# Optimization experiments

Measured on AMD Instinct MI355X. Metric: run time of the kernel, lower is better.

## Reference

```python
import jax, jax.numpy as jnp
import numpy as np

WS = 7   # window size
SS = 3   # shift size
NH = 8   # num heads


def _rel_pos_index(ws):
    coords = np.stack(np.meshgrid(np.arange(ws), np.arange(ws), indexing='ij')).reshape(2, -1)
    rel = (coords[:, :, None] - coords[:, None, :]).transpose(1, 2, 0)  # (N,N,2)
    rel[..., 0] += ws - 1
    rel[..., 1] += ws - 1
    rel[..., 0] *= 2 * ws - 1
    return rel.sum(-1)  # (N,N) int


def _shift_attn_mask(hp, wp, ws, ss):
    img = np.zeros((hp, wp), dtype=np.float32)
    sl = (slice(0, -ws), slice(-ws, -ss), slice(-ss, None))
    cnt = 0
    for hs in sl:
        for vs in sl:
            img[hs, vs] = cnt
            cnt += 1
    mw = img.reshape(hp // ws, ws, wp // ws, ws).transpose(0, 2, 1, 3).reshape(-1, ws * ws)
    diff = mw[:, None, :] - mw[:, :, None]  # (nW,N,N)
    return np.where(diff != 0, -100.0, 0.0).astype(np.float32)


def _window_partition(x, ws):
    b, h, w, c = x.shape
    x = x.reshape(b, h // ws, ws, w // ws, ws, c).transpose(0, 1, 3, 2, 4, 5)
    return x.reshape(-1, ws * ws, c)


def _window_reverse(win, h, w, ws, b):
    c = win.shape[-1]
    x = win.reshape(b, h // ws, w // ws, ws, ws, c).transpose(0, 1, 3, 2, 4, 5)
    return x.reshape(b, h, w, c)


def setup_inputs() -> dict:
    key = jax.random.key(0)
    ks = jax.random.split(key, 6)
    B, H, W, C = 16, 56, 56, 256
    return {
        'query': jax.random.normal(ks[0], (B, H * W, C), jnp.float32),
        'w_qkv': jax.random.normal(ks[1], (C, 3 * C), jnp.float32) * 0.02,
        'b_qkv': jax.random.normal(ks[2], (3 * C,), jnp.float32) * 0.02,
        'w_proj': jax.random.normal(ks[3], (C, C), jnp.float32) * 0.02,
        'b_proj': jax.random.normal(ks[4], (C,), jnp.float32) * 0.02,
        'rel_bias_table': jax.random.normal(ks[5], ((2 * WS - 1) ** 2, NH), jnp.float32) * 0.02,
        'height': H,
        'width': W,
    }


def reference(query, w_qkv, b_qkv, w_proj, b_proj, rel_bias_table, height, width):
    B, L, C = query.shape
    ws, ss, nh = WS, SS, NH
    hd = C // nh
    scale = hd ** -0.5
    x = query.reshape(B, height, width, C)

    pad_b = (ws - height % ws) % ws
    pad_r = (ws - width % ws) % ws
    x = jnp.pad(x, ((0, 0), (0, pad_b), (0, pad_r), (0, 0)))
    hp, wp = height + pad_b, width + pad_r

    # cyclic shift
    x = jnp.roll(x, (-ss, -ss), axis=(1, 2))
    attn_mask = jnp.asarray(_shift_attn_mask(hp, wp, ws, ss))  # (nW,N,N)

    win = _window_partition(x, ws)  # (B*nW, N, C)
    BW, N, _ = win.shape
    nW = (hp // ws) * (wp // ws)

    qkv = (win @ w_qkv + b_qkv).reshape(BW, N, 3, nh, hd).transpose(2, 0, 3, 1, 4)
    q, k, v = qkv[0], qkv[1], qkv[2]  # (BW, nh, N, hd)

    attn = jnp.einsum('bhnd,bhmd->bhnm', q * scale, k)  # (BW,nh,N,N)
    bias = rel_bias_table[_rel_pos_index(ws).reshape(-1)].reshape(N, N, nh).transpose(2, 0, 1)
    attn = attn + bias[None]
    attn = attn.reshape(B, nW, nh, N, N) + attn_mask[None, :, None]
    attn = jax.nn.softmax(attn.reshape(BW, nh, N, N), axis=-1)

    out = jnp.einsum('bhnm,bhmd->bhnd', attn, v).transpose(0, 2, 1, 3).reshape(BW, N, C)
    out = out @ w_proj + b_proj

    x = _window_reverse(out, hp, wp, ws, B)
    x = jnp.roll(x, (ss, ss), axis=(1, 2))
    x = x[:, :height, :width, :]
    return x.reshape(B, height * width, C)
```

## Files before the change

### kernel.cpp

```cpp
#include <hip/hip_runtime.h>


#define IMG 56
#define SCALE 0.17677669529663687f

typedef unsigned short u16;
typedef unsigned int u32;
typedef unsigned long long u64;
typedef __attribute__((ext_vector_type(8))) short short8;
typedef __attribute__((ext_vector_type(4))) float floatx4;

__device__ __forceinline__ float bflo(u32 u) { return __uint_as_float(u << 16); }
__device__ __forceinline__ u16 f2bf(float f) {
  u32 u = __float_as_uint(f);
  return (u16)((u + 0x7fffu + ((u >> 16) & 1u)) >> 16);
}
__device__ __forceinline__ u32 cvt2(float lo, float hi) {
  u32 r;
  __asm__("v_cvt_pk_bf16_f32 %0, %1, %2" : "=v"(r) : "v"(lo), "v"(hi));
  return r;
}
__device__ __forceinline__ short8 pack8(float4 lo, float4 hi) {
  union { u32 u[4]; short8 s; } r;
  r.u[0] = cvt2(lo.x, lo.y); r.u[1] = cvt2(lo.z, lo.w);
  r.u[2] = cvt2(hi.x, hi.y); r.u[3] = cvt2(hi.z, hi.w);
  return r.s;
}
#define MFMA(a, b, c) __builtin_amdgcn_mfma_f32_16x16x32_bf16(a, b, c, 0, 0, 0)

__device__ __forceinline__ void gll16(const void* g, const void* l) {
  __builtin_amdgcn_global_load_lds(
      (const __attribute__((address_space(1))) void*)g,
      (__attribute__((address_space(3))) void*)l, 16, 0, 0);
}
#define FENCE_VM() __asm__ volatile("s_waitcnt vmcnt(0)" ::: "memory")
#define FENCE_LGKM() __asm__ volatile("s_waitcnt lgkmcnt(0)" ::: "memory")

__device__ __forceinline__ int xcd_swizzle(int orig, int nwg) {
  int q = nwg >> 3, r = nwg & 7;
  int xcd = orig & 7, loc = orig >> 3;
  return (xcd < r ? xcd * (q + 1) : r * (q + 1) + (xcd - r) * q) + loc;
}

__global__ __launch_bounds__(256) void convert_kernel(
    const float* __restrict__ w_qkv, const float* __restrict__ w_proj,
    const float* __restrict__ bias_table, u16* __restrict__ zpad,
    u16* __restrict__ Wtq, u16* __restrict__ Wtp, u16* __restrict__ biasM) {
  int t = blockIdx.x * 256 + threadIdx.x;
  if (t < 196608) {
    int n = t % 768, k = t / 768;
    Wtq[n * 256 + k] = f2bf(w_qkv[t]);
  } else if (t < 262144) {
    int u = t - 196608;
    int n = u & 255, k = u >> 8;
    Wtp[n * 256 + k] = f2bf(w_proj[u]);
  } else if (t < 262272) {
    zpad[t - 262144] = 0;
  } else if (t < 393344) {
    int idx = t - 262272;
    int type = idx >> 15;
    int r = idx & 32767;
    int h = r >> 12, mt = (r >> 10) & 3, quad = (r >> 8) & 3;
    int l15 = (r >> 4) & 15, nt = (r >> 2) & 3, reg = r & 3;
    int row = 16 * mt + 4 * quad + reg;
    int col = 16 * nt + l15;
    float v;
    if (col >= 49) v = -1e30f;
    else if (row >= 49) v = 0.f;
    else {
      int yn = row / 7, xn = row - yn * 7;
      int ym = col / 7, xm = col - ym * 7;
      v = bias_table[((yn - ym + 6) * 13 + (xn - xm + 6)) * 8 + h];
      int bndH = (type >> 1) & 1, bndV = type & 1;
      int rc = (bndH ? ((yn < 4) ? 1 : 2) : 0) * 3 + (bndV ? ((xn < 4) ? 1 : 2) : 0);
      int cc = (bndH ? ((ym < 4) ? 1 : 2) : 0) * 3 + (bndV ? ((xm < 4) ? 1 : 2) : 0);
      if (rc != cc) v -= 100.f;
    }
    biasM[idx] = f2bf(v);
  }
}

__global__ __launch_bounds__(256) void qkv_gemm(
    const float* __restrict__ query, const u16* __restrict__ Wtq,
    const float* __restrict__ b_qkv, u16* __restrict__ QKVb,
    int img0, int Mrows, int mtiles) {
  union LU {
    struct { u16 As[128][64]; u16 Bs[128][64]; } s;
    u16 Cs[128][144];
  };
  __shared__ LU L;
  __shared__ float bqs[128];
  const int tid = threadIdx.x;
  const int wgid = xcd_swizzle(blockIdx.x, mtiles * 6);
  const int n0 = (wgid % 6) << 7;
  const int m0 = (wgid / 6) << 7;
  const int lane = tid & 63, w = tid >> 6;
  const int l15 = lane & 15, quad = lane >> 4;
  const int mq = w & 1, nq = w >> 1;
  if (tid < 128) bqs[tid] = b_qkv[n0 + tid];

  const float* qsrc[4];
  const u16* wsrc[4];
  #pragma unroll
  for (int c = 0; c < 4; ++c) {
    int e = (w * 4 + c) * 64 + lane;
    int row = e >> 3, sp = e & 7, sub = sp ^ (row & 7);
    int gr = m0 + row; if (gr >= Mrows) gr = 0;
    int winl = gr / 49, tok = gr - winl * 49;
    int bL = winl >> 6, wi = (winl >> 3) & 7, wj = winl & 7;
    int pr = tok / 7, pc = tok - pr * 7;
    int y = wi * 7 + pr + 3; if (y >= IMG) y -= IMG;
    int x = wj * 7 + pc + 3; if (x >= IMG) x -= IMG;
    qsrc[c] = query + (((size_t)((img0 + bL) * 3136 + y * IMG + x)) << 8) + sub * 8;
    wsrc[c] = Wtq + (size_t)(n0 + row) * 256 + sub * 8;
  }

  const floatx4 z4 = {0.f, 0.f, 0.f, 0.f};
  floatx4 acc[4][4];
  #pragma unroll
  for (int i = 0; i < 4; ++i)
    #pragma unroll
    for (int j = 0; j < 4; ++j) acc[i][j] = z4;

  float4 a0[4], a1[4];
  #pragma unroll
  for (int c = 0; c < 4; ++c) {
    a0[c] = reinterpret_cast<const float4*>(qsrc[c])[0];
    a1[c] = reinterpret_cast<const float4*>(qsrc[c])[1];
  }

  for (int ki = 0; ki < 4; ++ki) {
    const int k0 = ki * 64;
    __syncthreads();
    #pragma unroll
    for (int c = 0; c < 4; ++c)
      gll16(wsrc[c] + k0, (const char*)&L.s.Bs[0][0] + (w * 4 + c) * 1024);
    #pragma unroll
    for (int c = 0; c < 4; ++c) {
      short8 pk = pack8(a0[c], a1[c]);
      *reinterpret_cast<short8*>(
          (char*)&L.s.As[0][0] + (w * 4 + c) * 1024 + lane * 16) = pk;
    }
    FENCE_VM();
    __syncthreads();
    {
      const int kn = (ki < 3) ? k0 + 64 : 0;
      #pragma unroll
      for (int c = 0; c < 4; ++c) {
        const float* src = qsrc[c] + kn;
        a0[c] = reinterpret_cast<const float4*>(src)[0];
        a1[c] = reinterpret_cast<const float4*>(src)[1];
      }
    }
    #pragma unroll
    for (int ks = 0; ks < 2; ++ks) {
      short8 af[4], bfv[4];
      #pragma unroll
      for (int mt = 0; mt < 4; ++mt) {
        int r = 64 * mq + 16 * mt + l15;
        af[mt] = *reinterpret_cast<const short8*>(
            &L.s.As[r][((4 * ks + quad) ^ (l15 & 7)) * 8]);
      }
      #pragma unroll
      for (int nt = 0; nt < 4; ++nt) {
        int r = 64 * nq + 16 * nt + l15;
        bfv[nt] = *reinterpret_cast<const short8*>(
            &L.s.Bs[r][((4 * ks + quad) ^ (l15 & 7)) * 8]);
      }
      #pragma unroll
      for (int mt = 0; mt < 4; ++mt)
        #pragma unroll
        for (int nt = 0; nt < 4; ++nt)
          acc[mt][nt] = MFMA(af[mt], bfv[nt], acc[mt][nt]);
    }
  }
  __syncthreads();
  #pragma unroll
  for (int mt = 0; mt < 4; ++mt)
    #pragma unroll
    for (int nt = 0; nt < 4; ++nt) {
      float bias = bqs[64 * nq + 16 * nt + l15];
      #pragma unroll
      for (int reg = 0; reg < 4; ++reg) {
        int row = 64 * mq + 16 * mt + 4 * quad + reg;
        int col = 64 * nq + 16 * nt + l15;
        L.Cs[row][col] = f2bf(acc[mt][nt][reg] + bias);
      }
    }
  __syncthreads();
  int r = tid >> 1, half = tid & 1;
  if (m0 + r < Mrows) {
    u16* dst = QKVb + (size_t)(m0 + r) * 768 + n0 + half * 64;
    const u16* src = &L.Cs[r][half * 64];
    #pragma unroll
    for (int it = 0; it < 8; ++it)
      reinterpret_cast<uint4*>(dst)[it] = reinterpret_cast<const uint4*>(src)[it];
  }
}

__global__ __launch_bounds__(256) void attn_kernel(
    const u16* __restrict__ QKVb, const u16* __restrict__ biasM,
    const u16* __restrict__ zpad, u16* __restrict__ O) {
  __shared__ __align__(16) u16 wbuf[4][6144];
  const int tid = threadIdx.x;
  const int winl = blockIdx.x >> 1;
  const int hg = (blockIdx.x & 1) * 4;
  const int lane = tid & 63, w = tid >> 6;
  const int l15 = lane & 15, quad = lane >> 4;
  const int h = hg + w;
  const int wi = (winl >> 3) & 7;
  const int wj = winl & 7;
  const int type = ((wi == 7) ? 2 : 0) | ((wj == 7) ? 1 : 0);

  u16* wb = wbuf[w];
  const size_t wrow = (size_t)winl * 49;
  #pragma unroll
  for (int c = 0; c < 4; ++c) {
    int tok = c * 16 + (lane >> 2), sub = lane & 3;
    const u16 *gq, *gk;
    if (tok < 49) {
      const u16* g = QKVb + (wrow + tok) * 768 + h * 32 + sub * 8;
      gq = g; gk = g + 256;
    } else {
      gq = zpad + sub * 8; gk = zpad + sub * 8;
    }
    gll16(gq, (const char*)wb + c * 1024);
    gll16(gk, (const char*)wb + 4096 + c * 1024);
  }
  short8 v0 = {}, v1 = {}, v2 = {}, v3 = {};
  {
    int tok = lane;
    if (tok < 49) {
      const short8* g = reinterpret_cast<const short8*>(
          QKVb + (wrow + tok) * 768 + 512 + h * 32);
      v0 = g[0]; v1 = g[1]; v2 = g[2]; v3 = g[3];
    }
  }
  const u16* bb = biasM + ((((type << 3) + h) << 12) + (quad << 8) + (l15 << 4));
  short8 bf0[4], bf1[4];
  #pragma unroll
  for (int mt = 0; mt < 4; ++mt) {
    bf0[mt] = *reinterpret_cast<const short8*>(bb + (mt << 10));
    bf1[mt] = *reinterpret_cast<const short8*>(bb + (mt << 10) + 8);
  }
  {
    int tok = lane;
    #pragma unroll
    for (int d = 0; d < 8; ++d) {
      wb[4096 + (d     ) * 64 + tok] = (u16)v0[d];
      wb[4096 + (d +  8) * 64 + tok] = (u16)v1[d];
      wb[4096 + (d + 16) * 64 + tok] = (u16)v2[d];
      wb[4096 + (d + 24) * 64 + tok] = (u16)v3[d];
    }
  }
  FENCE_VM(); FENCE_LGKM();

  const floatx4 z4 = {0.f, 0.f, 0.f, 0.f};
  short8 qf[4], kf[4];
  #pragma unroll
  for (int mt = 0; mt < 4; ++mt)
    qf[mt] = *reinterpret_cast<const short8*>(&wb[(16 * mt + l15) * 32 + quad * 8]);
  #pragma unroll
  for (int nt = 0; nt < 4; ++nt)
    kf[nt] = *reinterpret_cast<const short8*>(&wb[2048 + (16 * nt + l15) * 32 + quad * 8]);
  floatx4 sc[4][4];
  #pragma unroll
  for (int mt = 0; mt < 4; ++mt)
    #pragma unroll
    for (int nt = 0; nt < 4; ++nt) sc[mt][nt] = MFMA(qf[mt], kf[nt], z4);

  #pragma unroll
  for (int mt = 0; mt < 4; ++mt)
    #pragma unroll
    for (int nt = 0; nt < 4; ++nt)
      #pragma unroll
      for (int reg = 0; reg < 4; ++reg) {
        u16 bv = (nt < 2) ? (u16)bf0[mt][(nt << 2) | reg]
                          : (u16)bf1[mt][((nt & 1) << 2) | reg];
        sc[mt][nt][reg] = sc[mt][nt][reg] * SCALE + bflo((u32)bv);
      }
  #pragma unroll
  for (int mt = 0; mt < 4; ++mt)
    #pragma unroll
    for (int reg = 0; reg < 4; ++reg) {
      float m = fmaxf(fmaxf(sc[mt][0][reg], sc[mt][1][reg]),
                      fmaxf(sc[mt][2][reg], sc[mt][3][reg]));
      m = fmaxf(m, __shfl_xor(m, 1)); m = fmaxf(m, __shfl_xor(m, 2));
      m = fmaxf(m, __shfl_xor(m, 4)); m = fmaxf(m, __shfl_xor(m, 8));
      float sum = 0.f;
      #pragma unroll
      for (int nt = 0; nt < 4; ++nt) {
        float e = __expf(sc[mt][nt][reg] - m);
        sc[mt][nt][reg] = e; sum += e;
      }
      sum += __shfl_xor(sum, 1); sum += __shfl_xor(sum, 2);
      sum += __shfl_xor(sum, 4); sum += __shfl_xor(sum, 8);
      float inv = 1.f / sum;
      #pragma unroll
      for (int nt = 0; nt < 4; ++nt) sc[mt][nt][reg] *= inv;
    }
  #pragma unroll
  for (int mt = 0; mt < 4; ++mt)
    #pragma unroll
    for (int nt = 0; nt < 4; ++nt)
      #pragma unroll
      for (int reg = 0; reg < 4; ++reg)
        wb[(16 * mt + 4 * quad + reg) * 64 + 16 * nt + l15] = f2bf(sc[mt][nt][reg]);
  FENCE_LGKM();
  floatx4 oa[4][2];
  #pragma unroll
  for (int mt = 0; mt < 4; ++mt) { oa[mt][0] = z4; oa[mt][1] = z4; }
  #pragma unroll
  for (int ks = 0; ks < 2; ++ks) {
    short8 pf[4], vf[2];
    #pragma unroll
    for (int mt = 0; mt < 4; ++mt)
      pf[mt] = *reinterpret_cast<const short8*>(
          &wb[(16 * mt + l15) * 64 + ks * 32 + quad * 8]);
    #pragma unroll
    for (int ntl = 0; ntl < 2; ++ntl)
      vf[ntl] = *reinterpret_cast<const short8*>(
          &wb[4096 + (16 * ntl + l15) * 64 + ks * 32 + quad * 8]);
    #pragma unroll
    for (int mt = 0; mt < 4; ++mt)
      #pragma unroll
      for (int ntl = 0; ntl < 2; ++ntl)
        oa[mt][ntl] = MFMA(pf[mt], vf[ntl], oa[mt][ntl]);
  }
  FENCE_LGKM();
  #pragma unroll
  for (int mt = 0; mt < 4; ++mt)
    #pragma unroll
    for (int ntl = 0; ntl < 2; ++ntl)
      #pragma unroll
      for (int reg = 0; reg < 4; ++reg)
        wb[4096 + (16 * mt + 4 * quad + reg) * 32 + 16 * ntl + l15] =
            f2bf(oa[mt][ntl][reg]);
  FENCE_LGKM();
  #pragma unroll
  for (int c = 0; c < 4; ++c) {
    int slot = c * 64 + lane;
    if (slot < 196) {
      int tok = slot >> 2, sub = slot & 3;
      uint4 v = *reinterpret_cast<const uint4*>(&wb[4096 + tok * 32 + sub * 8]);
      *reinterpret_cast<uint4*>(O + (wrow + tok) * 256 + h * 32 + sub * 8) = v;
    }
  }
}

__global__ __launch_bounds__(256) void proj_gemm(
    const u16* __restrict__ O, const u16* __restrict__ Wtp,
    const float* __restrict__ b_proj, float* __restrict__ out,
    int img0, int Mrows, int mtiles) {
  union LU {
    struct { u16 As[128][64]; u16 Bs[128][64]; } s;
    float Cs[64][132];
  };
  __shared__ LU L;
  __shared__ float bps[128];
  const int tid = threadIdx.x;
  const int wgid = xcd_swizzle(blockIdx.x, mtiles * 2);
  const int n0 = (wgid & 1) << 7;
  const int m0 = (wgid >> 1) << 7;
  const int lane = tid & 63, w = tid >> 6;
  const int l15 = lane & 15, quad = lane >> 4;
  const int mq = w & 1, nq = w >> 1;
  if (tid < 128) bps[tid] = b_proj[n0 + tid];

  const floatx4 z4 = {0.f, 0.f, 0.f, 0.f};
  floatx4 acc[4][4];
  #pragma unroll
  for (int i = 0; i < 4; ++i)
    #pragma unroll
    for (int j = 0; j < 4; ++j) acc[i][j] = z4;

  for (int ki = 0; ki < 4; ++ki) {
    const int k0 = ki * 64;
    __syncthreads();
    #pragma unroll
    for (int c = 0; c < 4; ++c) {
      int e = (w * 4 + c) * 64 + lane;
      int row = e >> 3, sp = e & 7, sub = sp ^ (row & 7);
      int gr = m0 + row; if (gr >= Mrows) gr = 0;
      gll16(O + (size_t)gr * 256 + k0 + sub * 8,
            (const char*)&L.s.As[0][0] + (w * 4 + c) * 1024);
      gll16(Wtp + (size_t)(n0 + row) * 256 + k0 + sub * 8,
            (const char*)&L.s.Bs[0][0] + (w * 4 + c) * 1024);
    }
    FENCE_VM();
    __syncthreads();
    #pragma unroll
    for (int ks = 0; ks < 2; ++ks) {
      short8 af[4], bfv[4];
      #pragma unroll
      for (int mt = 0; mt < 4; ++mt) {
        int r = 64 * mq + 16 * mt + l15;
        af[mt] = *reinterpret_cast<const short8*>(
            &L.s.As[r][((4 * ks + quad) ^ (l15 & 7)) * 8]);
      }
      #pragma unroll
      for (int nt = 0; nt < 4; ++nt) {
        int r = 64 * nq + 16 * nt + l15;
        bfv[nt] = *reinterpret_cast<const short8*>(
            &L.s.Bs[r][((4 * ks + quad) ^ (l15 & 7)) * 8]);
      }
      #pragma unroll
      for (int mt = 0; mt < 4; ++mt)
        #pragma unroll
        for (int nt = 0; nt < 4; ++nt)
          acc[mt][nt] = MFMA(af[mt], bfv[nt], acc[mt][nt]);
    }
  }
  #pragma unroll
  for (int mh = 0; mh < 2; ++mh) {
    __syncthreads();
    if (mq == mh) {
      #pragma unroll
      for (int nt = 0; nt < 4; ++nt) {
        float bias = bps[64 * nq + 16 * nt + l15];
        #pragma unroll
        for (int mt = 0; mt < 4; ++mt)
          #pragma unroll
          for (int reg = 0; reg < 4; ++reg)
            L.Cs[16 * mt + 4 * quad + reg][64 * nq + 16 * nt + l15] =
                acc[mt][nt][reg] + bias;
      }
    }
    __syncthreads();
    int r = tid >> 2, seg = tid & 3;
    int gr = m0 + mh * 64 + r;
    if (gr < Mrows) {
      u32 winl = (u32)gr / 49u;
      int tok = gr - (int)winl * 49;
      int bL = winl >> 6, wi = (winl >> 3) & 7, wj = winl & 7;
      int pr = tok / 7, pc = tok - pr * 7;
      int y = wi * 7 + pr + 3; if (y >= IMG) y -= IMG;
      int x = wj * 7 + pc + 3; if (x >= IMG) x -= IMG;
      float* op = out + (((size_t)((img0 + bL) * 3136 + y * IMG + x)) << 8) +
                  n0 + seg * 32;
      const float* src = &L.Cs[r][seg * 32];
      #pragma unroll
      for (int i = 0; i < 8; ++i)
        reinterpret_cast<float4*>(op)[i] = reinterpret_cast<const float4*>(src)[i];
    }
  }
}

extern "C" void kernel_launch(void* const* d_in, const int* in_sizes, int n_in,
                              void* d_out, int out_size, void* d_ws, size_t ws_size,
                              hipStream_t stream) {
  const float* query      = (const float*)d_in[0];
  const float* w_qkv      = (const float*)d_in[1];
  const float* b_qkv      = (const float*)d_in[2];
  const float* w_proj     = (const float*)d_in[3];
  const float* b_proj     = (const float*)d_in[4];
  const float* bias_table = (const float*)d_in[5];

  u16* wsu   = (u16*)d_ws;
  u16* zpad  = wsu;
  u16* Wtq   = wsu + 128;
  u16* Wtp   = wsu + 196736;
  u16* biasM = wsu + 262272;

  int P = 16;
  while (P > 1 && 2ull * (393344ull + (u64)P * 3211264ull) > (u64)ws_size) P >>= 1;
  u16* QKVb = wsu + 393344;
  u16* Ob   = QKVb + (size_t)P * 2408448;
  const int npass  = 16 / P;
  const int Mrows  = P * 3136;
  const int mtiles = (Mrows + 127) / 128;

  convert_kernel<<<1537, 256, 0, stream>>>(w_qkv, w_proj, bias_table,
                                           zpad, Wtq, Wtp, biasM);
  for (int p = 0; p < npass; ++p) {
    qkv_gemm<<<mtiles * 6, 256, 0, stream>>>(query, Wtq, b_qkv, QKVb,
                                             p * P, Mrows, mtiles);
    attn_kernel<<<P * 128, 256, 0, stream>>>(QKVb, biasM, zpad, Ob);
    proj_gemm<<<mtiles * 2, 256, 0, stream>>>(Ob, Wtp, b_proj, (float*)d_out,
                                              p * P, Mrows, mtiles);
  }
}
```

Before: 223.9 us.

## Double-buffer LDS tiles in QKV and projection GEMMs to overlap loads with MFMA

Both GEMM kernels now keep two LDS stages for the A and B tiles. The next K-slice is issued via global_load_lds (plus the packed fp32-to-bf16 query tile) before the MFMAs on the current slice run, with explicit waitcnt and raw s_barrier in place of two __syncthreads per iteration. The aim is to hide global load latency behind the matrix math. The cost is double the LDS footprint, which may lower occupancy, and hand-tuned vmcnt values that must match the exact number of outstanding loads.

Measured after the change: 226.7 us. Within noise of the previous version (+1.2%).

```diff
diff --git a/kernel.cpp b/kernel.cpp
--- a/kernel.cpp
+++ b/kernel.cpp
@@ -35,6 +35,12 @@
 }
 #define FENCE_VM() __asm__ volatile("s_waitcnt vmcnt(0)" ::: "memory")
 #define FENCE_LGKM() __asm__ volatile("s_waitcnt lgkmcnt(0)" ::: "memory")
+#define WAIT_VM8_LGKM0() \
+  __asm__ volatile("s_waitcnt vmcnt(8) lgkmcnt(0)" ::: "memory")
+#define WAIT_VM0_LGKM0() \
+  __asm__ volatile("s_waitcnt vmcnt(0) lgkmcnt(0)" ::: "memory")
+#define RAW_BARRIER() __asm__ volatile("s_barrier" ::: "memory")
+#define SCHED0() __builtin_amdgcn_sched_barrier(0)
 
 __device__ __forceinline__ int xcd_swizzle(int orig, int nwg) {
   int q = nwg >> 3, r = nwg & 7;
@@ -85,7 +91,7 @@
     const float* __restrict__ b_qkv, u16* __restrict__ QKVb,
     int img0, int Mrows, int mtiles) {
   union LU {
-    struct { u16 As[128][64]; u16 Bs[128][64]; } s;
+    struct { u16 As[2][128][64]; u16 Bs[2][128][64]; } s;
     u16 Cs[128][144];
   };
   __shared__ LU L;
@@ -114,6 +120,7 @@
     qsrc[c] = query + (((size_t)((img0 + bL) * 3136 + y * IMG + x)) << 8) + sub * 8;
     wsrc[c] = Wtq + (size_t)(n0 + row) * 256 + sub * 8;
   }
+  const int ldsoff = (w * 4) * 1024 + lane * 16;
 
   const floatx4 z4 = {0.f, 0.f, 0.f, 0.f};
   floatx4 acc[4][4];
@@ -128,29 +135,46 @@
     a0[c] = reinterpret_cast<const float4*>(qsrc[c])[0];
     a1[c] = reinterpret_cast<const float4*>(qsrc[c])[1];
   }
-
+  #pragma unroll
+  for (int c = 0; c < 4; ++c)
+    gll16(wsrc[c], (const char*)&L.s.Bs[0][0][0] + ldsoff - lane * 16 + c * 1024);
+  SCHED0();
+  #pragma unroll
+  for (int c = 0; c < 4; ++c)
+    *reinterpret_cast<short8*>(
+        (char*)&L.s.As[0][0][0] + ldsoff + c * 1024) = pack8(a0[c], a1[c]);
+  #pragma unroll
+  for (int c = 0; c < 4; ++c) {
+    const float* src = qsrc[c] + 64;
+    a0[c] = reinterpret_cast<const float4*>(src)[0];
+    a1[c] = reinterpret_cast<const float4*>(src)[1];
+  }
+  SCHED0();
+  WAIT_VM8_LGKM0();
+  RAW_BARRIER();
+
+  #pragma unroll
   for (int ki = 0; ki < 4; ++ki) {
-    const int k0 = ki * 64;
-    __syncthreads();
-    #pragma unroll
-    for (int c = 0; c < 4; ++c)
-      gll16(wsrc[c] + k0, (const char*)&L.s.Bs[0][0] + (w * 4 + c) * 1024);
-    #pragma unroll
-    for (int c = 0; c < 4; ++c) {
-      short8 pk = pack8(a0[c], a1[c]);
-      *reinterpret_cast<short8*>(
-          (char*)&L.s.As[0][0] + (w * 4 + c) * 1024 + lane * 16) = pk;
-    }
-    FENCE_VM();
-    __syncthreads();
-    {
-      const int kn = (ki < 3) ? k0 + 64 : 0;
-      #pragma unroll
-      for (int c = 0; c < 4; ++c) {
-        const float* src = qsrc[c] + kn;
-        a0[c] = reinterpret_cast<const float4*>(src)[0];
-        a1[c] = reinterpret_cast<const float4*>(src)[1];
-      }
+    const int cur = ki & 1, nxt = cur ^ 1;
+    if (ki < 3) {
+      #pragma unroll
+      for (int c = 0; c < 4; ++c)
+        gll16(wsrc[c] + (ki + 1) * 64,
+              (const char*)&L.s.Bs[nxt][0][0] + c * 1024 + (w * 4) * 1024);
+      SCHED0();
+      #pragma unroll
+      for (int c = 0; c < 4; ++c)
+        *reinterpret_cast<short8*>(
+            (char*)&L.s.As[nxt][0][0] + ldsoff + c * 1024) = pack8(a0[c], a1[c]);
+      if (ki < 2) {
+        #pragma unroll
+        for (int c = 0; c < 4; ++c) {
+          const float* src = qsrc[c] + (ki + 2) * 64;
+          a0[c] = reinterpret_cast<const float4*>(src)[0];
+          a1[c] = reinterpret_cast<const float4*>(src)[1];
+        }
+      }
+      SCHED0();
     }
     #pragma unroll
     for (int ks = 0; ks < 2; ++ks) {
@@ -159,19 +183,24 @@
       for (int mt = 0; mt < 4; ++mt) {
         int r = 64 * mq + 16 * mt + l15;
         af[mt] = *reinterpret_cast<const short8*>(
-            &L.s.As[r][((4 * ks + quad) ^ (l15 & 7)) * 8]);
+            &L.s.As[cur][r][((4 * ks + quad) ^ (l15 & 7)) * 8]);
       }
       #pragma unroll
       for (int nt = 0; nt < 4; ++nt) {
         int r = 64 * nq + 16 * nt + l15;
         bfv[nt] = *reinterpret_cast<const short8*>(
-            &L.s.Bs[r][((4 * ks + quad) ^ (l15 & 7)) * 8]);
+            &L.s.Bs[cur][r][((4 * ks + quad) ^ (l15 & 7)) * 8]);
       }
       #pragma unroll
       for (int mt = 0; mt < 4; ++mt)
         #pragma unroll
         for (int nt = 0; nt < 4; ++nt)
           acc[mt][nt] = MFMA(af[mt], bfv[nt], acc[mt][nt]);
+    }
+    if (ki < 3) {
+      if (ki < 2) WAIT_VM8_LGKM0();
+      else        WAIT_VM0_LGKM0();
+      RAW_BARRIER();
     }
   }
   __syncthreads();
@@ -353,7 +382,7 @@
     const float* __restrict__ b_proj, float* __restrict__ out,
     int img0, int Mrows, int mtiles) {
   union LU {
-    struct { u16 As[128][64]; u16 Bs[128][64]; } s;
+    struct { u16 As[2][128][64]; u16 Bs[2][128][64]; } s;
     float Cs[64][132];
   };
   __shared__ LU L;
@@ -367,6 +396,17 @@
   const int mq = w & 1, nq = w >> 1;
   if (tid < 128) bps[tid] = b_proj[n0 + tid];
 
+  const u16* asrc[4];
+  const u16* bsrc[4];
+  #pragma unroll
+  for (int c = 0; c < 4; ++c) {
+    int e = (w * 4 + c) * 64 + lane;
+    int row = e >> 3, sp = e & 7, sub = sp ^ (row & 7);
+    int gr = m0 + row; if (gr >= Mrows) gr = 0;
+    asrc[c] = O + (size_t)gr * 256 + sub * 8;
+    bsrc[c] = Wtp + (size_t)(n0 + row) * 256 + sub * 8;
+  }
+
   const floatx4 z4 = {0.f, 0.f, 0.f, 0.f};
   floatx4 acc[4][4];
   #pragma unroll
@@ -374,21 +414,27 @@
     #pragma unroll
     for (int j = 0; j < 4; ++j) acc[i][j] = z4;
 
+  #pragma unroll
+  for (int c = 0; c < 4; ++c) {
+    gll16(asrc[c], (const char*)&L.s.As[0][0][0] + (w * 4 + c) * 1024);
+    gll16(bsrc[c], (const char*)&L.s.Bs[0][0][0] + (w * 4 + c) * 1024);
+  }
+  SCHED0();
+  WAIT_VM0_LGKM0();
+  RAW_BARRIER();
+
+  #pragma unroll
   for (int ki = 0; ki < 4; ++ki) {
-    const int k0 = ki * 64;
-    __syncthreads();
-    #pragma unroll
-    for (int c = 0; c < 4; ++c) {
-      int e = (w * 4 + c) * 64 + lane;
-      int row = e >> 3, sp = e & 7, sub = sp ^ (row & 7);
-      int gr = m0 + row; if (gr >= Mrows) gr = 0;
-      gll16(O + (size_t)gr * 256 + k0 + sub * 8,
-            (const char*)&L.s.As[0][0] + (w * 4 + c) * 1024);
-      gll16(Wtp + (size_t)(n0 + row) * 256 + k0 + sub * 8,
-            (const char*)&L.s.Bs[0][0] + (w * 4 + c) * 1024);
-    }
-    FENCE_VM();
-    __syncthreads();
+    const int cur = ki & 1, nxt = cur ^ 1;
+    if (ki < 3) {
+      const int kn = (ki + 1) * 64;
+      #pragma unroll
+      for (int c = 0; c < 4; ++c) {
+        gll16(asrc[c] + kn, (const char*)&L.s.As[nxt][0][0] + (w * 4 + c) * 1024);
+        gll16(bsrc[c] + kn, (const char*)&L.s.Bs[nxt][0][0] + (w * 4 + c) * 1024);
+      }
+      SCHED0();
+    }
     #pragma unroll
     for (int ks = 0; ks < 2; ++ks) {
       short8 af[4], bfv[4];
@@ -396,19 +442,23 @@
       for (int mt = 0; mt < 4; ++mt) {
         int r = 64 * mq + 16 * mt + l15;
         af[mt] = *reinterpret_cast<const short8*>(
-            &L.s.As[r][((4 * ks + quad) ^ (l15 & 7)) * 8]);
+            &L.s.As[cur][r][((4 * ks + quad) ^ (l15 & 7)) * 8]);
       }
       #pragma unroll
       for (int nt = 0; nt < 4; ++nt) {
         int r = 64 * nq + 16 * nt + l15;
         bfv[nt] = *reinterpret_cast<const short8*>(
-            &L.s.Bs[r][((4 * ks + quad) ^ (l15 & 7)) * 8]);
+            &L.s.Bs[cur][r][((4 * ks + quad) ^ (l15 & 7)) * 8]);
       }
       #pragma unroll
       for (int mt = 0; mt < 4; ++mt)
         #pragma unroll
         for (int nt = 0; nt < 4; ++nt)
           acc[mt][nt] = MFMA(af[mt], bfv[nt], acc[mt][nt]);
+    }
+    if (ki < 3) {
+      WAIT_VM0_LGKM0();
+      RAW_BARRIER();
     }
   }
   #pragma unroll
```
